# Performance work log

Hardware: AMD Instinct MI355X
Metric: run time of the kernel (lower is better)

Reference implementation:

```python
import jax, jax.numpy as jnp
import numpy as np

B, T, C, HS = 8, 2048, 1024, 64


def setup_inputs() -> dict:
    key = jax.random.key(0)
    kx, kq, kk, kv = jax.random.split(key, 4)
    x = jax.random.normal(kx, (B, T, C), dtype=jnp.float32)
    # torch Linear(C, HS, bias=False): weight [HS, C], y = x @ W.T -> store as [C, HS]
    Wq = jax.random.normal(kq, (C, HS), dtype=jnp.float32) * (C ** -0.5)
    Wk = jax.random.normal(kk, (C, HS), dtype=jnp.float32) * (C ** -0.5)
    Wv = jax.random.normal(kv, (C, HS), dtype=jnp.float32) * (C ** -0.5)
    return {"x": x, "Wq": Wq, "Wk": Wk, "Wv": Wv}


def reference(x, Wq, Wk, Wv):
    _, t, c = x.shape
    q = jnp.einsum('btc,ch->bth', x, Wq)
    k = jnp.einsum('btc,ch->bth', x, Wk)
    v = jnp.einsum('btc,ch->bth', x, Wv)
    # NOTE: original scales by C**-0.5 (hidden_dim), not head_size**-0.5
    scores = jnp.einsum('bth,bsh->bts', q, k) * (c ** -0.5)  # [B,T,T]
    causal = jnp.tril(jnp.ones((t, t), dtype=bool))
    scores = jnp.where(causal, scores, -jnp.inf)
    probs = jax.nn.softmax(scores, axis=-1)  # dropout p=0.0 -> identity
    out = jnp.einsum('bts,bsh->bth', probs, v)  # [B,T,HS]
    return out
```

## Files before the change

kernel.cpp:

```cpp
#include <hip/hip_runtime.h>
#include <hip/hip_bf16.h>

#define B_ 8
#define T_ 2048
#define C_ 1024
#define HS_ 64

typedef float f32x4 __attribute__((ext_vector_type(4)));
typedef __bf16 bf16x8 __attribute__((ext_vector_type(8)));
typedef __bf16 bf16x4 __attribute__((ext_vector_type(4)));

__device__ __forceinline__ void gld_lds16(const void* g, void* l) {
    __builtin_amdgcn_global_load_lds(
        (const __attribute__((address_space(1))) void*)g,
        (__attribute__((address_space(3))) void*)l, 16, 0, 0);
}


__global__ __launch_bounds__(256) void wt_kernel(const float* __restrict__ Wq,
                                                 const float* __restrict__ Wk,
                                                 const float* __restrict__ Wv,
                                                 __bf16* __restrict__ wt) {
    __shared__ float tile[64][65];
    int mb = blockIdx.x >> 4;
    int k0 = (blockIdx.x & 15) * 64;
    const float* W = (mb == 0) ? Wq : (mb == 1 ? Wk : Wv);
    int c = threadIdx.x & 63;
#pragma unroll
    for (int r = threadIdx.x >> 6; r < 64; r += 4)
        tile[r][c] = W[(size_t)(k0 + r) * 64 + c];
    __syncthreads();
    float scale = (mb == 0) ? (0.03125f * 1.44269504f) : 1.0f;
    int kk = threadIdx.x & 63;
#pragma unroll
    for (int n = threadIdx.x >> 6; n < 64; n += 4) {
        int col = (((kk >> 3) ^ (n & 7)) * 8) + (kk & 7);
        wt[(size_t)(mb * 64 + n) * C_ + k0 + col] = (__bf16)(tile[kk][n] * scale);
    }
}

__global__ __launch_bounds__(512) void qkv_kernel(const float* __restrict__ x,
                                                  const __bf16* __restrict__ wt,
                                                  __bf16* __restrict__ qf,
                                                  __bf16* __restrict__ kf,
                                                  __bf16* __restrict__ vf) {
    __shared__ __align__(16) char smem[57344];
    __bf16* xs0 = (__bf16*)smem;
    __bf16* xs1 = (__bf16*)(smem + 4096);
    __bf16* ws0 = (__bf16*)(smem + 8192);
    __bf16* ws1 = (__bf16*)(smem + 32768);

    const int tid = threadIdx.x;
    const int w = tid >> 6, lane = tid & 63, lq = lane & 15, lg = lane >> 4;
    const int m0 = blockIdx.x * 32;
    const int mt = w & 1;
    const int ntb = (w >> 1) * 3;

    f32x4 acc[3];
#pragma unroll
    for (int i = 0; i < 3; ++i) acc[i] = (f32x4)0.0f;

    const int xrow = tid >> 3, xch = tid & 7;
    float4 xr0, xr1;
    const int wslot0 = w * 3 * 64 + lane;

    if (tid < 256) {
        const float* xp = x + (size_t)(m0 + xrow) * C_ + xch * 8;
        xr0 = *(const float4*)xp;
        xr1 = *(const float4*)(xp + 4);
    }
#pragma unroll
    for (int s = 0; s < 3; ++s) {
        int slot = wslot0 + s * 64;
        gld_lds16(wt + (size_t)(slot >> 3) * C_ + (slot & 7) * 8,
                  ws0 + (w * 3 + s) * 512);
    }
    if (tid < 256) {
        bf16x8 xb;
#pragma unroll
        for (int j = 0; j < 4; ++j) { xb[j] = (__bf16)xr0[j]; xb[4 + j] = (__bf16)xr1[j]; }
        *(bf16x8*)(xs0 + xrow * 64 + ((xch ^ (xrow & 7)) * 8)) = xb;
    }

    for (int kt = 0; kt < 16; ++kt) {
        __syncthreads();
        __bf16* xsc = (kt & 1) ? xs1 : xs0;
        __bf16* wsc = (kt & 1) ? ws1 : ws0;
        __bf16* xsn = (kt & 1) ? xs0 : xs1;
        __bf16* wsn = (kt & 1) ? ws0 : ws1;
        if (kt < 15) {
            int k0 = (kt + 1) * 64;
            if (tid < 256) {
                const float* xp = x + (size_t)(m0 + xrow) * C_ + k0 + xch * 8;
                xr0 = *(const float4*)xp;
                xr1 = *(const float4*)(xp + 4);
            }
#pragma unroll
            for (int s = 0; s < 3; ++s) {
                int slot = wslot0 + s * 64;
                gld_lds16(wt + (size_t)(slot >> 3) * C_ + k0 + (slot & 7) * 8,
                          wsn + (w * 3 + s) * 512);
            }
        }
#pragma unroll
        for (int ks = 0; ks < 2; ++ks) {
            int r = mt * 16 + lq;
            bf16x8 a = *(const bf16x8*)(xsc + r * 64 + (((ks * 4 + lg) ^ (r & 7)) * 8));
#pragma unroll
            for (int i = 0; i < 3; ++i) {
                int rw = (ntb + i) * 16 + lq;
                bf16x8 b = *(const bf16x8*)(wsc + rw * 64 + (((ks * 4 + lg) ^ (rw & 7)) * 8));
                acc[i] = __builtin_amdgcn_mfma_f32_16x16x32_bf16(a, b, acc[i], 0, 0, 0);
            }
        }
        if (kt < 15 && tid < 256) {
            bf16x8 xb;
#pragma unroll
            for (int j = 0; j < 4; ++j) { xb[j] = (__bf16)xr0[j]; xb[4 + j] = (__bf16)xr1[j]; }
            *(bf16x8*)(xsn + xrow * 64 + ((xch ^ (xrow & 7)) * 8)) = xb;
        }
    }
    __syncthreads();

    __bf16(*obuf)[208] = (__bf16(*)[208])smem;
#pragma unroll
    for (int i = 0; i < 3; ++i)
#pragma unroll
        for (int r = 0; r < 4; ++r)
            obuf[mt * 16 + lg * 4 + r][(ntb + i) * 16 + lq] = (__bf16)acc[i][r];
    __syncthreads();

    if (w < 4) {
        int mg = w & 1, half = w >> 1;
        size_t qt16 = (size_t)(m0 >> 4) + mg;
        bf16x8 vq = *(const bf16x8*)&obuf[mg * 16 + lq][half * 32 + lg * 8];
        bf16x8 vk = *(const bf16x8*)&obuf[mg * 16 + lq][64 + half * 32 + lg * 8];
        *(bf16x8*)(qf + ((qt16 * 2 + half) * 64 + lane) * 8) = vq;
        *(bf16x8*)(kf + ((qt16 * 2 + half) * 64 + lane) * 8) = vk;
    } else {
        int ntv = w - 4;
        bf16x8 vv;
#pragma unroll
        for (int j = 0; j < 8; ++j)
            vv[j] = obuf[lg * 8 + j][128 + ntv * 16 + lq];
        size_t kt32 = (size_t)(m0 >> 5);
        *(bf16x8*)(vf + ((kt32 * 4 + ntv) * 64 + lane) * 8) = vv;
    }
}

__global__ __launch_bounds__(512, 4) void attn_kernel(const __bf16* __restrict__ qf,
                                                      const __bf16* __restrict__ kf,
                                                      const __bf16* __restrict__ vf,
                                                      float* __restrict__ out) {
    __shared__ float olds[8][16][64];
    __shared__ float mlds[8][16], llds[8][16];
    __shared__ __align__(16) __bf16 plds[8][16 * 72];

    int w    = threadIdx.x >> 6;
    int lane = threadIdx.x & 63;
    int lq = lane & 15, lg = lane >> 4;

    int b  = blockIdx.x & 7;
    int q0 = (63 - (blockIdx.x >> 3)) * 32;
    int qs = w >> 2;
    int wk = w & 3;
    int qt = q0 + qs * 16;

    size_t qbase = ((size_t)b * 128 + (qt >> 4)) * 2;
    bf16x8 aq0 = *(const bf16x8*)(qf + ((qbase + 0) * 64 + lane) * 8);
    bf16x8 aq1 = *(const bf16x8*)(qf + ((qbase + 1) * 64 + lane) * 8);

    f32x4 o[4];
#pragma unroll
    for (int nt = 0; nt < 4; ++nt) o[nt] = (f32x4)0.0f;
    float m_s = -1e30f, l_s = 0.f;

    __bf16* pw = &plds[w][0];

    int ntiles = (qt + 79) >> 6;
    for (int kt = wk; kt < ntiles; kt += 4) {
        int s0 = kt * 64;
        f32x4 s[4];
        __builtin_amdgcn_s_setprio(1);
#pragma unroll
        for (int ct = 0; ct < 4; ++ct) {
            size_t kbase = ((size_t)b * 128 + (s0 >> 4) + ct) * 2;
            bf16x8 k0 = *(const bf16x8*)(kf + ((kbase + 0) * 64 + lane) * 8);
            bf16x8 k1 = *(const bf16x8*)(kf + ((kbase + 1) * 64 + lane) * 8);
            f32x4 a = (f32x4)0.0f;
            a = __builtin_amdgcn_mfma_f32_16x16x32_bf16(k0, aq0, a, 0, 0, 0);
            a = __builtin_amdgcn_mfma_f32_16x16x32_bf16(k1, aq1, a, 0, 0, 0);
            s[ct] = a;
        }
        __builtin_amdgcn_s_setprio(0);
        if (s0 + 63 > qt) {
#pragma unroll
            for (int ct = 0; ct < 4; ++ct)
#pragma unroll
                for (int r = 0; r < 4; ++r)
                    if (s0 + ct * 16 + lg * 4 + r > qt + lq) s[ct][r] = -1e30f;
        }
        bf16x8 bv[2][4];
#pragma unroll
        for (int ks = 0; ks < 2; ++ks)
#pragma unroll
            for (int nt = 0; nt < 4; ++nt)
                bv[ks][nt] = *(const bf16x8*)(vf +
                    (((size_t)(b * 64 + (s0 >> 5) + ks) * 4 + nt) * 64 + lane) * 8);
        float pm = -1e30f;
#pragma unroll
        for (int ct = 0; ct < 4; ++ct)
#pragma unroll
            for (int r = 0; r < 4; ++r) pm = fmaxf(pm, s[ct][r]);
        pm = fmaxf(pm, __shfl_xor(pm, 16));
        pm = fmaxf(pm, __shfl_xor(pm, 32));
        bool need = __any(pm > m_s);
        float al = 1.0f;
        if (need) {
            float mn = fmaxf(m_s, pm);
            al = exp2f(m_s - mn);
            m_s = mn;
        }
        float rs = 0.f;
        f32x4 p[4];
#pragma unroll
        for (int ct = 0; ct < 4; ++ct)
#pragma unroll
            for (int r = 0; r < 4; ++r) {
                p[ct][r] = exp2f(s[ct][r] - m_s);
                rs += p[ct][r];
            }
        rs += __shfl_xor(rs, 16);
        rs += __shfl_xor(rs, 32);
        if (need) {
            l_s = l_s * al + rs;
            float alr[4];
#pragma unroll
            for (int r = 0; r < 4; ++r) alr[r] = __shfl(al, lg * 4 + r);
#pragma unroll
            for (int nt = 0; nt < 4; ++nt)
#pragma unroll
                for (int r = 0; r < 4; ++r) o[nt][r] *= alr[r];
        } else {
            l_s += rs;
        }
#pragma unroll
        for (int ct = 0; ct < 4; ++ct) {
            bf16x4 qv;
#pragma unroll
            for (int r = 0; r < 4; ++r) qv[r] = (__bf16)p[ct][r];
            *(bf16x4*)&pw[lq * 72 + ct * 16 + lg * 4] = qv;
        }
        asm volatile("" ::: "memory");
        bf16x8 pa0 = *(const bf16x8*)&pw[lq * 72 + lg * 8];
        bf16x8 pa1 = *(const bf16x8*)&pw[lq * 72 + 32 + lg * 8];
        __builtin_amdgcn_s_setprio(1);
#pragma unroll
        for (int nt = 0; nt < 4; ++nt) {
            o[nt] = __builtin_amdgcn_mfma_f32_16x16x32_bf16(pa0, bv[0][nt], o[nt], 0, 0, 0);
            o[nt] = __builtin_amdgcn_mfma_f32_16x16x32_bf16(pa1, bv[1][nt], o[nt], 0, 0, 0);
        }
        __builtin_amdgcn_s_setprio(0);
    }

    asm volatile("" ::: "memory");
#pragma unroll
    for (int nt = 0; nt < 4; ++nt)
#pragma unroll
        for (int r = 0; r < 4; ++r)
            olds[w][lg * 4 + r][nt * 16 + lq] = o[nt][r];
    if (lg == 0) {
        mlds[w][lq] = m_s;
        llds[w][lq] = l_s;
    }
    __syncthreads();

    int row = threadIdx.x >> 4;
    int c4  = (threadIdx.x & 15) * 4;
    int wb  = (row >> 4) * 4;
    int r16 = row & 15;
    float M = -1e30f;
#pragma unroll
    for (int w2 = 0; w2 < 4; ++w2) M = fmaxf(M, mlds[wb + w2][r16]);
    float L = 0.f;
    f32x4 oa = (f32x4)0.0f;
#pragma unroll
    for (int w2 = 0; w2 < 4; ++w2) {
        float sc = exp2f(mlds[wb + w2][r16] - M);
        L += sc * llds[wb + w2][r16];
        const float* op = &olds[wb + w2][r16][c4];
#pragma unroll
        for (int j = 0; j < 4; ++j) oa[j] += sc * op[j];
    }
    float inv = 1.0f / L;
    float4 st;
    st.x = oa[0] * inv; st.y = oa[1] * inv; st.z = oa[2] * inv; st.w = oa[3] * inv;
    *(float4*)(out + ((size_t)b * T_ + q0 + row) * HS_ + c4) = st;
}

extern "C" void kernel_launch(void* const* d_in, const int* in_sizes, int n_in,
                              void* d_out, int out_size, void* d_ws, size_t ws_size,
                              hipStream_t stream) {
    const float* x  = (const float*)d_in[0];
    const float* Wq = (const float*)d_in[1];
    const float* Wk = (const float*)d_in[2];
    const float* Wv = (const float*)d_in[3];
    char* ws = (char*)d_ws;
    __bf16* wt = (__bf16*)ws;
    __bf16* qf = (__bf16*)(ws + 393216);
    __bf16* kf = (__bf16*)(ws + 2490368);
    __bf16* vf = (__bf16*)(ws + 4587520);
    float* out = (float*)d_out;

    wt_kernel<<<dim3(48), dim3(256), 0, stream>>>(Wq, Wk, Wv, wt);
    qkv_kernel<<<dim3(512), dim3(512), 0, stream>>>(x, wt, qf, kf, vf);
    attn_kernel<<<dim3(512), dim3(512), 0, stream>>>(qf, kf, vf, out);
}
```

Baseline: 40.77 us.

## Restructure attention to stage K/V tiles in LDS with double-buffered async loads

The attention kernel changes from 512-thread blocks, where 4 waves split the key range and merge partial softmax results through LDS, to 256-thread blocks of 64 query rows. Each wave owns 16 rows and walks every key tile. K and V tiles are staged cooperatively into double-buffered LDS with global_load_lds, so the 4 waves share them instead of each wave loading its own from global memory. The cross-wave merge and its final sync are removed, and the output is normalized and written directly. In exchange the grid shrinks to 256 blocks with more serial work per wave, so load balance and occupancy on the CUs may drop.

```diff
diff --git a/kernel.cpp b/kernel.cpp
--- a/kernel.cpp
+++ b/kernel.cpp
@@ -148,23 +148,17 @@
     }
 }
 
-__global__ __launch_bounds__(512, 4) void attn_kernel(const __bf16* __restrict__ qf,
-                                                      const __bf16* __restrict__ kf,
-                                                      const __bf16* __restrict__ vf,
-                                                      float* __restrict__ out) {
-    __shared__ float olds[8][16][64];
-    __shared__ float mlds[8][16], llds[8][16];
-    __shared__ __align__(16) __bf16 plds[8][16 * 72];
-
-    int w    = threadIdx.x >> 6;
-    int lane = threadIdx.x & 63;
-    int lq = lane & 15, lg = lane >> 4;
-
-    int b  = blockIdx.x & 7;
-    int q0 = (63 - (blockIdx.x >> 3)) * 32;
-    int qs = w >> 2;
-    int wk = w & 3;
-    int qt = q0 + qs * 16;
+__global__ __launch_bounds__(256) void attn_kernel(const __bf16* __restrict__ qf,
+                                                   const __bf16* __restrict__ kf,
+                                                   const __bf16* __restrict__ vf,
+                                                   float* __restrict__ out) {
+    __shared__ __align__(16) char smem[41984];
+
+    const int tid = threadIdx.x;
+    const int w = tid >> 6, lane = tid & 63, lq = lane & 15, lg = lane >> 4;
+    const int b  = blockIdx.x & 7;
+    const int q0 = (31 - (blockIdx.x >> 3)) * 64;
+    const int qt = q0 + w * 16;
 
     size_t qbase = ((size_t)b * 128 + (qt >> 4)) * 2;
     bf16x8 aq0 = *(const bf16x8*)(qf + ((qbase + 0) * 64 + lane) * 8);
@@ -175,18 +169,40 @@
     for (int nt = 0; nt < 4; ++nt) o[nt] = (f32x4)0.0f;
     float m_s = -1e30f, l_s = 0.f;
 
-    __bf16* pw = &plds[w][0];
-
-    int ntiles = (qt + 79) >> 6;
-    for (int kt = wk; kt < ntiles; kt += 4) {
+    __bf16* pw = (__bf16*)(smem + 32768 + w * 2304);
+
+    const int ntiles = (q0 >> 6) + 1;
+
+#define STAGE(T, DST)                                                          \
+    {                                                                          \
+        int s0_ = (T) * 64;                                                    \
+        const __bf16* ks_ = kf + ((size_t)b * 128 + (s0_ >> 4)) * 1024;        \
+        const __bf16* vs_ = vf + ((size_t)b * 64 + (s0_ >> 5)) * 2048;         \
+        gld_lds16(ks_ + (size_t)tid * 8,         (DST) + tid * 16);            \
+        gld_lds16(ks_ + (size_t)(tid + 256) * 8, (DST) + (tid + 256) * 16);    \
+        gld_lds16(vs_ + (size_t)tid * 8,         (DST) + 8192 + tid * 16);     \
+        gld_lds16(vs_ + (size_t)(tid + 256) * 8, (DST) + 8192 + (tid + 256) * 16); \
+    }
+
+    STAGE(0, smem);
+
+    for (int kt = 0; kt < ntiles; ++kt) {
+        __syncthreads();
+        char* cbuf = smem + (kt & 1) * 16384;
+        if (kt + 1 < ntiles) {
+            char* nbuf = smem + ((kt + 1) & 1) * 16384;
+            STAGE(kt + 1, nbuf);
+        }
+        const __bf16* kb = (const __bf16*)cbuf;
+        const __bf16* vb = (const __bf16*)(cbuf + 8192);
         int s0 = kt * 64;
+
         f32x4 s[4];
         __builtin_amdgcn_s_setprio(1);
 #pragma unroll
         for (int ct = 0; ct < 4; ++ct) {
-            size_t kbase = ((size_t)b * 128 + (s0 >> 4) + ct) * 2;
-            bf16x8 k0 = *(const bf16x8*)(kf + ((kbase + 0) * 64 + lane) * 8);
-            bf16x8 k1 = *(const bf16x8*)(kf + ((kbase + 1) * 64 + lane) * 8);
+            bf16x8 k0 = *(const bf16x8*)(kb + (ct * 2 + 0) * 512 + lane * 8);
+            bf16x8 k1 = *(const bf16x8*)(kb + (ct * 2 + 1) * 512 + lane * 8);
             f32x4 a = (f32x4)0.0f;
             a = __builtin_amdgcn_mfma_f32_16x16x32_bf16(k0, aq0, a, 0, 0, 0);
             a = __builtin_amdgcn_mfma_f32_16x16x32_bf16(k1, aq1, a, 0, 0, 0);
@@ -200,13 +216,6 @@
                 for (int r = 0; r < 4; ++r)
                     if (s0 + ct * 16 + lg * 4 + r > qt + lq) s[ct][r] = -1e30f;
         }
-        bf16x8 bv[2][4];
-#pragma unroll
-        for (int ks = 0; ks < 2; ++ks)
-#pragma unroll
-            for (int nt = 0; nt < 4; ++nt)
-                bv[ks][nt] = *(const bf16x8*)(vf +
-                    (((size_t)(b * 64 + (s0 >> 5) + ks) * 4 + nt) * 64 + lane) * 8);
         float pm = -1e30f;
 #pragma unroll
         for (int ct = 0; ct < 4; ++ct)
@@ -257,45 +266,25 @@
         __builtin_amdgcn_s_setprio(1);
 #pragma unroll
         for (int nt = 0; nt < 4; ++nt) {
-            o[nt] = __builtin_amdgcn_mfma_f32_16x16x32_bf16(pa0, bv[0][nt], o[nt], 0, 0, 0);
-            o[nt] = __builtin_amdgcn_mfma_f32_16x16x32_bf16(pa1, bv[1][nt], o[nt], 0, 0, 0);
+            bf16x8 bv0 = *(const bf16x8*)(vb + (0 * 4 + nt) * 512 + lane * 8);
+            o[nt] = __builtin_amdgcn_mfma_f32_16x16x32_bf16(pa0, bv0, o[nt], 0, 0, 0);
+            bf16x8 bv1 = *(const bf16x8*)(vb + (1 * 4 + nt) * 512 + lane * 8);
+            o[nt] = __builtin_amdgcn_mfma_f32_16x16x32_bf16(pa1, bv1, o[nt], 0, 0, 0);
         }
         __builtin_amdgcn_s_setprio(0);
     }
-
-    asm volatile("" ::: "memory");
+#undef STAGE
+
+    float rcp = 1.0f / l_s;
+    float inv[4];
+#pragma unroll
+    for (int r = 0; r < 4; ++r) inv[r] = __shfl(rcp, lg * 4 + r);
+    float* ob = out + ((size_t)b * T_ + qt) * HS_;
 #pragma unroll
     for (int nt = 0; nt < 4; ++nt)
 #pragma unroll
         for (int r = 0; r < 4; ++r)
-            olds[w][lg * 4 + r][nt * 16 + lq] = o[nt][r];
-    if (lg == 0) {
-        mlds[w][lq] = m_s;
-        llds[w][lq] = l_s;
-    }
-    __syncthreads();
-
-    int row = threadIdx.x >> 4;
-    int c4  = (threadIdx.x & 15) * 4;
-    int wb  = (row >> 4) * 4;
-    int r16 = row & 15;
-    float M = -1e30f;
-#pragma unroll
-    for (int w2 = 0; w2 < 4; ++w2) M = fmaxf(M, mlds[wb + w2][r16]);
-    float L = 0.f;
-    f32x4 oa = (f32x4)0.0f;
-#pragma unroll
-    for (int w2 = 0; w2 < 4; ++w2) {
-        float sc = exp2f(mlds[wb + w2][r16] - M);
-        L += sc * llds[wb + w2][r16];
-        const float* op = &olds[wb + w2][r16][c4];
-#pragma unroll
-        for (int j = 0; j < 4; ++j) oa[j] += sc * op[j];
-    }
-    float inv = 1.0f / L;
-    float4 st;
-    st.x = oa[0] * inv; st.y = oa[1] * inv; st.z = oa[2] * inv; st.w = oa[3] * inv;
-    *(float4*)(out + ((size_t)b * T_ + q0 + row) * HS_ + c4) = st;
+            ob[(size_t)(lg * 4 + r) * HS_ + nt * 16 + lq] = o[nt][r] * inv[r];
 }
 
 extern "C" void kernel_launch(void* const* d_in, const int* in_sizes, int n_in,
@@ -314,5 +303,5 @@
 
     wt_kernel<<<dim3(48), dim3(256), 0, stream>>>(Wq, Wk, Wv, wt);
     qkv_kernel<<<dim3(512), dim3(512), 0, stream>>>(x, wt, qf, kf, vf);
-    attn_kernel<<<dim3(512), dim3(512), 0, stream>>>(qf, kf, vf, out);
-}
+    attn_kernel<<<dim3(256), dim3(256), 0, stream>>>(qf, kf, vf, out);
+}
```

After: 63.89 us. 1.57x slower.
